# Kernel optimization log

Measured on AMD Instinct MI355X. Metric: run time of the kernel, lower is better.

## Reference

```python
import jax, jax.numpy as jnp
import numpy as np

K = 16  # neighbors


def _knn_idx(pts, k):
    # pts: [B,N,3] -> idx [B,N,K] of k nearest points (self included), unsorted order ok
    sq = jnp.sum(pts * pts, axis=-1)                                  # [B,N]
    d = sq[:, :, None] + sq[:, None, :] - 2.0 * jnp.einsum('bnd,bmd->bnm', pts, pts)
    return jax.lax.top_k(-d, k)[1]                                    # [B,N,K]


def _gather(x, idx):
    # x: [B,N,C], idx: [B,N,K] -> [B,N,K,C]
    return jax.vmap(lambda xb, ib: xb[ib])(x, idx)


def _lin(x, W, b):
    # pointwise (kernel-1 conv / linear): x [...,Cin], W [Cout,Cin]
    return jnp.einsum('...c,oc->...o', x, W) + b


def _local_maxpool(x, idx):
    return jnp.max(_gather(x, idx), axis=2)                           # [B,N,C]


def setup_inputs() -> dict:
    key = jax.random.key(0)
    ks = jax.random.split(key, 24)
    B, N = 8, 4096

    def p(k, shape):
        fan_in = shape[-1]
        return jax.random.normal(k, shape, jnp.float32) * (1.0 / np.sqrt(fan_in))

    z = lambda n: jnp.zeros((n,), jnp.float32)
    return {
        'pts': jax.random.normal(ks[0], (B, N, 3), jnp.float32),
        'w1': p(ks[1], (64, 12)),    'b1': z(64),
        'w2': p(ks[2], (64, 64)),    'b2': z(64),
        'w3': p(ks[3], (64, 64)),    'b3': z(64),
        'lw1': p(ks[4], (64, 64)),   'lb1': z(64),
        'cw1': p(ks[5], (128, 64)),  'cb1': z(128),
        'lw2': p(ks[6], (128, 128)), 'lb2': z(128),
        'cw2': p(ks[7], (1024, 128)),'cb2': z(1024),
        'mw1': p(ks[8], (512, 1024)),'mb1': z(512),
        'mw2': p(ks[9], (512, 512)), 'mb2': z(512),
    }


def reference(pts, w1, b1, w2, b2, w3, b3, lw1, lb1, cw1, cb1,
              lw2, lb2, cw2, cb2, mw1, mb1, mw2, mb2):
    B, N, d = pts.shape
    idx = _knn_idx(pts, K)                                            # [B,N,K]

    # local covariance: gather neighbors, center, outer-product sum
    nb = _gather(pts, idx)                                            # [B,N,K,3]
    nb = nb - jnp.mean(nb, axis=2, keepdims=True)
    cov = jnp.einsum('bnki,bnkj->bnij', nb, nb).reshape(B, N, d * d)  # [B,N,9]
    x = jnp.concatenate([pts, cov], axis=-1)                          # [B,N,12]

    # mlp1 (three 1x1 convs + relu)
    x = jax.nn.relu(_lin(x, w1, b1))
    x = jax.nn.relu(_lin(x, w2, b2))
    x = jax.nn.relu(_lin(x, w3, b3))                                  # [B,N,64]

    # graph layer
    x = _local_maxpool(x, idx)
    x = _lin(x, lw1, lb1)
    x = jax.nn.relu(_lin(x, cw1, cb1))                                # [B,N,128]
    x = _local_maxpool(x, idx)
    x = _lin(x, lw2, lb2)
    x = _lin(x, cw2, cb2)                                             # [B,N,1024]

    # global max pool over points, then mlp2
    x = jnp.max(x, axis=1, keepdims=True)                             # [B,1,1024]
    x = jax.nn.relu(_lin(x, mw1, mb1))
    x = _lin(x, mw2, mb2)                                             # [B,1,512]
    return x
```

## Files before the change

### kernel.cpp

```cpp
#include <hip/hip_runtime.h>

#define NPTS 4096
#define NBATCH 8

typedef __attribute__((ext_vector_type(8))) short short8v;
typedef __attribute__((ext_vector_type(4))) float f32x4;

__device__ __forceinline__ unsigned fenc(float f) {
  unsigned u = __float_as_uint(f);
  return (u & 0x80000000u) ? ~u : (u | 0x80000000u);
}
__device__ __forceinline__ float fdec(unsigned e) {
  unsigned u = (e & 0x80000000u) ? (e ^ 0x80000000u) : ~e;
  return __uint_as_float(u);
}
__device__ __forceinline__ float dot4(float4 a, float4 b) {
  return a.x * b.x + a.y * b.y + a.z * b.z + a.w * b.w;
}
__device__ __forceinline__ unsigned short f2bf(float f) {
  unsigned u = __float_as_uint(f);
  return (unsigned short)((u + 0x7fffu + ((u >> 16) & 1u)) >> 16);
}

__global__ __launch_bounds__(256)
void k_wb(const float* __restrict__ cw2, unsigned short* __restrict__ cw2B) {
  int tid = blockIdx.x * 256 + threadIdx.x;
  int l = tid & 63, ks = (tid >> 6) & 3, nt = tid >> 8;
  int n = nt * 16 + (l & 15);
  int kb = ks * 32 + (l >> 4) * 8;
  const float* src = cw2 + (size_t)n * 128 + kb;
  unsigned short* dst = cw2B + (size_t)tid * 8;
#pragma unroll
  for (int j = 0; j < 8; j++) dst[j] = f2bf(src[j]);
}

__global__ __launch_bounds__(256)
void k_pack(const float* __restrict__ pts, float4* __restrict__ pts4) {
  int i = blockIdx.x * 256 + threadIdx.x;
  float x = pts[3 * i], y = pts[3 * i + 1], z = pts[3 * i + 2];
  pts4[i] = make_float4(x, y, z, x * x + y * y + z * z);
}

__global__ __launch_bounds__(512)
void k_knn(const float4* __restrict__ pts4, int* __restrict__ idxo,
           float* __restrict__ x0) {
  __shared__ float bufd[16][512];
  __shared__ unsigned short bufi[16][512];

  const int b = blockIdx.x >> 6;
  const int ch = blockIdx.x & 63;
  const float4* pb4 = pts4 + (size_t)b * NPTS;

  const int t = threadIdx.x;
  const int tq = t & 63;
  const int seg = __builtin_amdgcn_readfirstlane(t >> 6);
  const int q = ch * 64 + tq;
  const float4 qp = pb4[q];
  const float qs = qp.w;

  float td[16];
  int ti[16];
#pragma unroll
  for (int j = 0; j < 16; j++) { td[j] = 3.0e38f; ti[j] = 0; }
  float worst = 3.0e38f;
  int cnt = 0;

  auto merge = [&]() {
    float bd[16];
    int bi[16];
#pragma unroll
    for (int j = 0; j < 16; j++) {
      bool v = j < cnt;
      float dv = bufd[j][t];
      int iv = (int)bufi[j][t];
      bd[j] = v ? dv : 3.0e38f;
      bi[j] = v ? iv : 0;
    }
    cnt = 0;
#pragma unroll
    for (int k = 2; k <= 16; k <<= 1) {
#pragma unroll
      for (int j = k >> 1; j > 0; j >>= 1) {
#pragma unroll
        for (int i = 0; i < 16; i++) {
          int l = i ^ j;
          if (l > i) {
            bool dir = ((i & k) == 0);
            bool sw = dir ? (bd[i] > bd[l]) : (bd[i] < bd[l]);
            float fd = sw ? bd[l] : bd[i];
            float fl = sw ? bd[i] : bd[l];
            int gd = sw ? bi[l] : bi[i];
            int gl = sw ? bi[i] : bi[l];
            bd[i] = fd; bd[l] = fl; bi[i] = gd; bi[l] = gl;
          }
        }
      }
    }
#pragma unroll
    for (int i = 0; i < 16; i++) {
      int l = 15 - i;
      bool sw = bd[l] < td[i];
      td[i] = sw ? bd[l] : td[i];
      ti[i] = sw ? bi[l] : ti[i];
    }
#pragma unroll
    for (int j = 8; j > 0; j >>= 1) {
#pragma unroll
      for (int i = 0; i < 16; i++) {
        int l = i ^ j;
        if (l > i) {
          bool sw = td[i] > td[l];
          float fd = sw ? td[l] : td[i];
          float fl = sw ? td[i] : td[l];
          int gd = sw ? ti[l] : ti[i];
          int gl = sw ? ti[i] : ti[l];
          td[i] = fd; td[l] = fl; ti[i] = gd; ti[l] = gl;
        }
      }
    }
    worst = td[15];
  };

  const float4* ps = pb4 + seg * 512;
  const int base = seg * 512;
  for (int i0 = 0; i0 < 512; i0 += 8) {
    float4 c[8];
#pragma unroll
    for (int u = 0; u < 8; u++) c[u] = ps[i0 + u];
    float d[8];
#pragma unroll
    for (int u = 0; u < 8; u++)
      d[u] = (qs + c[u].w) - 2.0f * (qp.x * c[u].x + qp.y * c[u].y + qp.z * c[u].z);
#pragma unroll
    for (int u = 0; u < 8; u++) {
      if (d[u] < worst) {
        bufd[cnt][t] = d[u];
        bufi[cnt][t] = (unsigned short)(base + i0 + u);
        cnt++;
      }
      if (u == 3 && __any(cnt >= 13)) merge();
    }
    if (__any(cnt >= 13)) merge();
  }
  if (__any(cnt > 0)) merge();

#pragma unroll
  for (int j = 0; j < 16; j++) { bufd[j][t] = td[j]; bufi[j][t] = (unsigned short)ti[j]; }
  __syncthreads();
  if (t < 64) {
#pragma unroll
    for (int s = 1; s < 8; s++) {
      float bd[16];
      int bi[16];
#pragma unroll
      for (int j = 0; j < 16; j++) {
        bd[j] = bufd[j][t + 64 * s];
        bi[j] = (int)bufi[j][t + 64 * s];
      }
#pragma unroll
      for (int i = 0; i < 16; i++) {
        int l = 15 - i;
        bool sw = bd[l] < td[i];
        td[i] = sw ? bd[l] : td[i];
        ti[i] = sw ? bi[l] : ti[i];
      }
#pragma unroll
      for (int j = 8; j > 0; j >>= 1) {
#pragma unroll
        for (int i = 0; i < 16; i++) {
          int l = i ^ j;
          if (l > i) {
            bool sw2 = td[i] > td[l];
            float fd = sw2 ? td[l] : td[i];
            float fl = sw2 ? td[i] : td[l];
            int gd = sw2 ? ti[l] : ti[i];
            int gl = sw2 ? ti[i] : ti[l];
            td[i] = fd; td[l] = fl; ti[i] = gd; ti[l] = gl;
          }
        }
      }
    }

    float nx[16], ny[16], nz[16];
    float mx = 0.f, my = 0.f, mz = 0.f;
#pragma unroll
    for (int k = 0; k < 16; k++) {
      float4 c = pb4[ti[k]];
      nx[k] = c.x; ny[k] = c.y; nz[k] = c.z;
      mx += c.x; my += c.y; mz += c.z;
    }
    mx *= 0.0625f; my *= 0.0625f; mz *= 0.0625f;
    float c00 = 0, c01 = 0, c02 = 0, c11 = 0, c12 = 0, c22 = 0;
#pragma unroll
    for (int k = 0; k < 16; k++) {
      float dx = nx[k] - mx, dy = ny[k] - my, dz = nz[k] - mz;
      c00 += dx * dx; c01 += dx * dy; c02 += dx * dz;
      c11 += dy * dy; c12 += dy * dz; c22 += dz * dz;
    }
    size_t row = (size_t)b * NPTS + q;
    float* xo = x0 + row * 12;
    xo[0] = qp.x; xo[1] = qp.y; xo[2] = qp.z;
    xo[3] = c00;  xo[4] = c01;  xo[5] = c02;
    xo[6] = c01;  xo[7] = c11;  xo[8] = c12;
    xo[9] = c02;  xo[10] = c12; xo[11] = c22;
    int* io = idxo + row * 16;
#pragma unroll
    for (int k = 0; k < 16; k++) io[k] = ti[k];
  }
}

__global__ __launch_bounds__(128)
void k_mlp1(const float* __restrict__ x0,
            const float* __restrict__ w1, const float* __restrict__ b1,
            const float* __restrict__ w2, const float* __restrict__ b2,
            const float* __restrict__ w3, const float* __restrict__ b3,
            float* __restrict__ h3o) {
  __shared__ float s1[64 * 12], s2[64 * 64], s3[64 * 64];
  __shared__ float sb1[64], sb2[64], sb3[64];
  for (int i = threadIdx.x; i < 64 * 12; i += 128) s1[i] = w1[i];
  for (int i = threadIdx.x; i < 64 * 64; i += 128) { s2[i] = w2[i]; s3[i] = w3[i]; }
  if (threadIdx.x < 64) {
    sb1[threadIdx.x] = b1[threadIdx.x];
    sb2[threadIdx.x] = b2[threadIdx.x];
    sb3[threadIdx.x] = b3[threadIdx.x];
  }
  __syncthreads();

  size_t p = (size_t)blockIdx.x * 128 + threadIdx.x;
  const float4* xv = (const float4*)(x0 + p * 12);
  float4 xa = xv[0], xb = xv[1], xc = xv[2];

  float h[64];
#pragma unroll
  for (int o = 0; o < 64; o++) {
    const float4* wr = (const float4*)(s1 + o * 12);
    float a = sb1[o] + dot4(wr[0], xa) + dot4(wr[1], xb) + dot4(wr[2], xc);
    h[o] = fmaxf(a, 0.f);
  }
  float g[64];
#pragma unroll
  for (int o = 0; o < 64; o++) {
    float a = sb2[o];
    const float4* wr = (const float4*)(s2 + o * 64);
#pragma unroll
    for (int c4 = 0; c4 < 16; c4++) {
      float4 w = wr[c4];
      a += w.x * h[4 * c4] + w.y * h[4 * c4 + 1] + w.z * h[4 * c4 + 2] + w.w * h[4 * c4 + 3];
    }
    g[o] = fmaxf(a, 0.f);
  }
  float* out = h3o + p * 64;
  for (int o = 0; o < 64; o++) {
    float a = sb3[o];
    const float4* wr = (const float4*)(s3 + o * 64);
#pragma unroll
    for (int c4 = 0; c4 < 16; c4++) {
      float4 w = wr[c4];
      a += w.x * g[4 * c4] + w.y * g[4 * c4 + 1] + w.z * g[4 * c4 + 2] + w.w * g[4 * c4 + 3];
    }
    out[o] = fmaxf(a, 0.f);
  }
}

__global__ __launch_bounds__(256)
void k_graph1(const float* __restrict__ h3, const int* __restrict__ idx,
              const float* __restrict__ lw1, const float* __restrict__ lb1,
              const float* __restrict__ cw1, const float* __restrict__ cb1,
              float* __restrict__ z) {
  __shared__ float smc[64][64];
  __shared__ float yc[64][64];

  const int b = blockIdx.x >> 6;
  const int pbase = (blockIdx.x & 63) * 64;
  const int t = threadIdx.x;
  const int pl = t & 63;
  const int cg = __builtin_amdgcn_readfirstlane(t >> 6);

  {
    size_t p = (size_t)b * NPTS + pbase + pl;
    const int* ip = idx + p * 16;
    float mv[16];
#pragma unroll
    for (int c = 0; c < 16; c++) mv[c] = -3.0e38f;
    for (int k = 0; k < 16; k++) {
      const float4* nb = (const float4*)(h3 + (((size_t)b << 12) + ip[k]) * 64 + cg * 16);
#pragma unroll
      for (int c4 = 0; c4 < 4; c4++) {
        float4 v = nb[c4];
        mv[4 * c4]     = fmaxf(mv[4 * c4], v.x);
        mv[4 * c4 + 1] = fmaxf(mv[4 * c4 + 1], v.y);
        mv[4 * c4 + 2] = fmaxf(mv[4 * c4 + 2], v.z);
        mv[4 * c4 + 3] = fmaxf(mv[4 * c4 + 3], v.w);
      }
    }
#pragma unroll
    for (int c = 0; c < 16; c++) smc[cg * 16 + c][pl] = mv[c];
  }
  __syncthreads();

  {
    float m[64];
#pragma unroll
    for (int c = 0; c < 64; c++) m[c] = smc[c][pl];
    for (int j = 0; j < 16; j++) {
      const float* wr = lw1 + (size_t)(cg * 16 + j) * 64;
      float a = lb1[cg * 16 + j];
#pragma unroll
      for (int c = 0; c < 64; c++) a += wr[c] * m[c];
      yc[cg * 16 + j][pl] = a;
    }
  }
  __syncthreads();

  {
    float y[64];
#pragma unroll
    for (int c = 0; c < 64; c++) y[c] = yc[c][pl];
    size_t p = (size_t)b * NPTS + pbase + pl;
    float* zo = z + p * 128 + cg * 32;
    for (int o4 = 0; o4 < 8; o4++) {
      float r[4];
#pragma unroll
      for (int oi = 0; oi < 4; oi++) {
        int o = o4 * 4 + oi;
        const float* wr = cw1 + (size_t)(cg * 32 + o) * 64;
        float a = cb1[cg * 32 + o];
#pragma unroll
        for (int c = 0; c < 64; c++) a += wr[c] * y[c];
        r[oi] = fmaxf(a, 0.f);
      }
      *(float4*)(zo + o4 * 4) = make_float4(r[0], r[1], r[2], r[3]);
    }
  }
}

__global__ __launch_bounds__(256)
void k_graph2(const float* __restrict__ z, const int* __restrict__ idx,
              const float* __restrict__ lw2, const float* __restrict__ lb2,
              const unsigned short* __restrict__ cw2B, const float* __restrict__ cb2,
              unsigned* __restrict__ gacc) {
  __shared__ float smT[128][64];
  __shared__ alignas(16) unsigned short stb[64 * 128];

  const int b = blockIdx.x >> 6;
  const int pbase = (blockIdx.x & 63) * 64;
  const int t = threadIdx.x;

  {
    const int pl = t & 63, cg = t >> 6;
    size_t p = (size_t)b * NPTS + pbase + pl;
    const int* ip = idx + p * 16;
    float mv[32];
#pragma unroll
    for (int c = 0; c < 32; c++) mv[c] = -3.0e38f;
    for (int k = 0; k < 16; k++) {
      const float4* nb = (const float4*)(z + ((size_t)b * NPTS + ip[k]) * 128 + cg * 32);
#pragma unroll
      for (int c4 = 0; c4 < 8; c4++) {
        float4 v = nb[c4];
        mv[4 * c4]     = fmaxf(mv[4 * c4], v.x);
        mv[4 * c4 + 1] = fmaxf(mv[4 * c4 + 1], v.y);
        mv[4 * c4 + 2] = fmaxf(mv[4 * c4 + 2], v.z);
        mv[4 * c4 + 3] = fmaxf(mv[4 * c4 + 3], v.w);
      }
    }
#pragma unroll
    for (int c = 0; c < 32; c++) smT[cg * 32 + c][pl] = mv[c];
  }
  __syncthreads();

  {
    const int pl = t & 63, og = t >> 6;
    float acc[32];
#pragma unroll
    for (int oi = 0; oi < 32; oi++) acc[oi] = lb2[og * 32 + oi];
    for (int cb = 0; cb < 4; cb++) {
      float mr[32];
#pragma unroll
      for (int j = 0; j < 32; j++) mr[j] = smT[cb * 32 + j][pl];
#pragma unroll
      for (int oi = 0; oi < 32; oi++) {
        const float4* wr = (const float4*)(lw2 + (size_t)(og * 32 + oi) * 128 + cb * 32);
#pragma unroll
        for (int j4 = 0; j4 < 8; j4++) {
          float4 w = wr[j4];
          acc[oi] += w.x * mr[4 * j4] + w.y * mr[4 * j4 + 1] + w.z * mr[4 * j4 + 2] + w.w * mr[4 * j4 + 3];
        }
      }
    }
#pragma unroll
    for (int e = 0; e < 4; e++) {
      short8v v;
#pragma unroll
      for (int j = 0; j < 8; j++) v[j] = (short)f2bf(acc[e * 8 + j]);
      int bc = (og * 64 + e * 16) ^ ((pl & 7) << 4);
      *(short8v*)((char*)stb + pl * 256 + bc) = v;
    }
  }
  __syncthreads();

  {
    const int wv = t >> 6;
    const int l = t & 63;
    const int lr = l & 15;
    const int lg = l >> 4;
    short8v a[4][4];
#pragma unroll
    for (int mt = 0; mt < 4; mt++)
#pragma unroll
      for (int ks = 0; ks < 4; ks++) {
        int row = mt * 16 + lr;
        int bc = (ks * 64 + lg * 16) ^ ((row & 7) << 4);
        a[mt][ks] = *(const short8v*)((const char*)stb + row * 256 + bc);
      }
    const short8v* cb8 = (const short8v*)cw2B;
    float bmax[16];
#pragma unroll
    for (int i = 0; i < 16; i++) {
      const int nt = wv * 16 + i;
      short8v bf[4];
#pragma unroll
      for (int ks = 0; ks < 4; ks++) bf[ks] = cb8[(nt * 4 + ks) * 64 + l];
      float mm = -3.0e38f;
#pragma unroll
      for (int mt = 0; mt < 4; mt++) {
        f32x4 acc = {0.f, 0.f, 0.f, 0.f};
#pragma unroll
        for (int ks = 0; ks < 4; ks++)
          acc = __builtin_amdgcn_mfma_f32_16x16x32_bf16(a[mt][ks], bf[ks], acc, 0, 0, 0);
        mm = fmaxf(mm, fmaxf(fmaxf(acc[0], acc[1]), fmaxf(acc[2], acc[3])));
      }
      mm = fmaxf(mm, __shfl_xor(mm, 16));
      mm = fmaxf(mm, __shfl_xor(mm, 32));
      bmax[i] = mm + cb2[nt * 16 + lr];
    }
    if (l < 16) {
#pragma unroll
      for (int i = 0; i < 16; i++)
        atomicMax(&gacc[b * 1024 + (wv * 16 + i) * 16 + l], fenc(bmax[i]));
    }
  }
}

__global__ __launch_bounds__(512)
void k_head(const unsigned* __restrict__ gacc,
            const float* __restrict__ mw1, const float* __restrict__ mb1,
            const float* __restrict__ mw2, const float* __restrict__ mb2,
            float* __restrict__ out) {
  __shared__ float g[1024];
  __shared__ float h[512];
  const int b = blockIdx.x, t = threadIdx.x;
  for (int i = t; i < 1024; i += 512) g[i] = fdec(gacc[b * 1024 + i]);
  __syncthreads();
  float a = mb1[t];
  const float4* wr = (const float4*)(mw1 + (size_t)t * 1024);
  const float4* gv = (const float4*)g;
#pragma unroll 8
  for (int c4 = 0; c4 < 256; c4++) a += dot4(wr[c4], gv[c4]);
  h[t] = fmaxf(a, 0.f);
  __syncthreads();
  float a2 = mb2[t];
  const float4* wr2 = (const float4*)(mw2 + (size_t)t * 512);
  const float4* hv = (const float4*)h;
#pragma unroll 8
  for (int c4 = 0; c4 < 128; c4++) a2 += dot4(wr2[c4], hv[c4]);
  out[(size_t)b * 512 + t] = a2;
}

extern "C" void kernel_launch(void* const* d_in, const int* in_sizes, int n_in,
                              void* d_out, int out_size, void* d_ws, size_t ws_size,
                              hipStream_t stream) {
  const float* pts = (const float*)d_in[0];
  const float* w1  = (const float*)d_in[1];
  const float* b1  = (const float*)d_in[2];
  const float* w2  = (const float*)d_in[3];
  const float* b2  = (const float*)d_in[4];
  const float* w3  = (const float*)d_in[5];
  const float* b3  = (const float*)d_in[6];
  const float* lw1 = (const float*)d_in[7];
  const float* lb1 = (const float*)d_in[8];
  const float* cw1 = (const float*)d_in[9];
  const float* cb1 = (const float*)d_in[10];
  const float* lw2 = (const float*)d_in[11];
  const float* lb2 = (const float*)d_in[12];
  const float* cw2 = (const float*)d_in[13];
  const float* cb2 = (const float*)d_in[14];
  const float* mw1 = (const float*)d_in[15];
  const float* mb1 = (const float*)d_in[16];
  const float* mw2 = (const float*)d_in[17];
  const float* mb2 = (const float*)d_in[18];

  char* ws = (char*)d_ws;
  int*      idx  = (int*)(ws);
  float*    x0   = (float*)(ws + 2097152);
  float*    h3   = (float*)(ws + 2097152 + 1572864);
  float*    z    = (float*)(ws + 2097152 + 1572864 + 8388608);
  unsigned* gacc = (unsigned*)(ws + 28835840);
  unsigned short* cw2B = (unsigned short*)(ws + 28835840 + 32768);
  float4*   pts4 = (float4*)(ws + 28835840 + 32768 + 262144);

  hipMemsetAsync(gacc, 0, NBATCH * 1024 * sizeof(unsigned), stream);
  k_wb<<<64, 256, 0, stream>>>(cw2, cw2B);
  k_pack<<<(NBATCH * NPTS) / 256, 256, 0, stream>>>(pts, pts4);
  k_knn<<<NBATCH * (NPTS / 64), 512, 0, stream>>>(pts4, idx, x0);
  k_mlp1<<<(NBATCH * NPTS) / 128, 128, 0, stream>>>(x0, w1, b1, w2, b2, w3, b3, h3);
  k_graph1<<<NBATCH * 64, 256, 0, stream>>>(h3, idx, lw1, lb1, cw1, cb1, z);
  k_graph2<<<NBATCH * (NPTS / 64), 256, 0, stream>>>(z, idx, lw2, lb2, cw2B, cb2, gacc);
  k_head<<<NBATCH, 512, 0, stream>>>(gacc, mw1, mb1, mw2, mb2, (float*)d_out);
}
```

Baseline: 507.0 us.

## Restructure mlp1 into block-cooperative layers and split head across more blocks

The per-point MLP1 kernel now has each block handle 64 points, with 4 waves each computing 16 output channels. Intermediate activations are staged in shared memory and weights are read through wave-uniform global loads, which cuts per-thread register arrays and redundant LDS weight copies. The MLP head, previously 8 blocks each doing a serial 1024-long dot product per thread, is split into two kernels over 64 blocks each. These use transposed weights for coalesced reads and an 8-way partial-sum reduction. This raises parallelism in the tiny head stage but adds two transpose launches and an extra head launch on every call.

```diff
diff --git a/kernel.cpp b/kernel.cpp
--- a/kernel.cpp
+++ b/kernel.cpp
@@ -39,6 +39,13 @@
   int i = blockIdx.x * 256 + threadIdx.x;
   float x = pts[3 * i], y = pts[3 * i + 1], z = pts[3 * i + 2];
   pts4[i] = make_float4(x, y, z, x * x + y * y + z * z);
+}
+
+__global__ __launch_bounds__(256)
+void k_trh(const float* __restrict__ src, float* __restrict__ dst, int cin) {
+  int idx = blockIdx.x * 256 + threadIdx.x;
+  int c = idx >> 9, o = idx & 511;
+  dst[idx] = src[o * cin + c];
 }
 
 __global__ __launch_bounds__(512)
@@ -209,56 +216,76 @@
   }
 }
 
-__global__ __launch_bounds__(128)
+__global__ __launch_bounds__(256)
 void k_mlp1(const float* __restrict__ x0,
             const float* __restrict__ w1, const float* __restrict__ b1,
             const float* __restrict__ w2, const float* __restrict__ b2,
             const float* __restrict__ w3, const float* __restrict__ b3,
             float* __restrict__ h3o) {
-  __shared__ float s1[64 * 12], s2[64 * 64], s3[64 * 64];
-  __shared__ float sb1[64], sb2[64], sb3[64];
-  for (int i = threadIdx.x; i < 64 * 12; i += 128) s1[i] = w1[i];
-  for (int i = threadIdx.x; i < 64 * 64; i += 128) { s2[i] = w2[i]; s3[i] = w3[i]; }
-  if (threadIdx.x < 64) {
-    sb1[threadIdx.x] = b1[threadIdx.x];
-    sb2[threadIdx.x] = b2[threadIdx.x];
-    sb3[threadIdx.x] = b3[threadIdx.x];
-  }
-  __syncthreads();
-
-  size_t p = (size_t)blockIdx.x * 128 + threadIdx.x;
-  const float4* xv = (const float4*)(x0 + p * 12);
-  float4 xa = xv[0], xb = xv[1], xc = xv[2];
-
-  float h[64];
-#pragma unroll
-  for (int o = 0; o < 64; o++) {
-    const float4* wr = (const float4*)(s1 + o * 12);
-    float a = sb1[o] + dot4(wr[0], xa) + dot4(wr[1], xb) + dot4(wr[2], xc);
-    h[o] = fmaxf(a, 0.f);
-  }
-  float g[64];
-#pragma unroll
-  for (int o = 0; o < 64; o++) {
-    float a = sb2[o];
-    const float4* wr = (const float4*)(s2 + o * 64);
-#pragma unroll
-    for (int c4 = 0; c4 < 16; c4++) {
-      float4 w = wr[c4];
-      a += w.x * h[4 * c4] + w.y * h[4 * c4 + 1] + w.z * h[4 * c4 + 2] + w.w * h[4 * c4 + 3];
-    }
-    g[o] = fmaxf(a, 0.f);
-  }
-  float* out = h3o + p * 64;
-  for (int o = 0; o < 64; o++) {
-    float a = sb3[o];
-    const float4* wr = (const float4*)(s3 + o * 64);
-#pragma unroll
-    for (int c4 = 0; c4 < 16; c4++) {
-      float4 w = wr[c4];
-      a += w.x * g[4 * c4] + w.y * g[4 * c4 + 1] + w.z * g[4 * c4 + 2] + w.w * g[4 * c4 + 3];
-    }
-    out[o] = fmaxf(a, 0.f);
+  __shared__ float xs[12][64];
+  __shared__ float h1[64][64];
+  __shared__ float h2[64][64];
+
+  const int b = blockIdx.x >> 6;
+  const int pbase = (blockIdx.x & 63) * 64;
+  const int t = threadIdx.x;
+  const int pl = t & 63;
+  const int cg = __builtin_amdgcn_readfirstlane(t >> 6);
+
+  {
+    const float* xt = x0 + ((size_t)b * NPTS + pbase) * 12;
+    for (int e = t; e < 768; e += 256) xs[e % 12][e / 12] = xt[e];
+  }
+  __syncthreads();
+
+  {
+    float x[12];
+#pragma unroll
+    for (int c = 0; c < 12; c++) x[c] = xs[c][pl];
+    for (int j = 0; j < 16; j++) {
+      int o = cg * 16 + j;
+      const float* wr = w1 + (size_t)o * 12;
+      float a = b1[o];
+#pragma unroll
+      for (int c = 0; c < 12; c++) a += wr[c] * x[c];
+      h1[o][pl] = fmaxf(a, 0.f);
+    }
+  }
+  __syncthreads();
+
+  {
+    float m[64];
+#pragma unroll
+    for (int c = 0; c < 64; c++) m[c] = h1[c][pl];
+    for (int j = 0; j < 16; j++) {
+      int o = cg * 16 + j;
+      const float* wr = w2 + (size_t)o * 64;
+      float a = b2[o];
+#pragma unroll
+      for (int c = 0; c < 64; c++) a += wr[c] * m[c];
+      h2[o][pl] = fmaxf(a, 0.f);
+    }
+  }
+  __syncthreads();
+
+  {
+    float m[64];
+#pragma unroll
+    for (int c = 0; c < 64; c++) m[c] = h2[c][pl];
+    float* out = h3o + ((size_t)b * NPTS + pbase + pl) * 64 + cg * 16;
+    for (int j4 = 0; j4 < 4; j4++) {
+      float r[4];
+#pragma unroll
+      for (int ji = 0; ji < 4; ji++) {
+        int o = cg * 16 + j4 * 4 + ji;
+        const float* wr = w3 + (size_t)o * 64;
+        float a = b3[o];
+#pragma unroll
+        for (int c = 0; c < 64; c++) a += wr[c] * m[c];
+        r[ji] = fmaxf(a, 0.f);
+      }
+      *(float4*)(out + j4 * 4) = make_float4(r[0], r[1], r[2], r[3]);
+    }
   }
 }
 
@@ -443,28 +470,55 @@
 }
 
 __global__ __launch_bounds__(512)
-void k_head(const unsigned* __restrict__ gacc,
-            const float* __restrict__ mw1, const float* __restrict__ mb1,
-            const float* __restrict__ mw2, const float* __restrict__ mb2,
-            float* __restrict__ out) {
-  __shared__ float g[1024];
-  __shared__ float h[512];
-  const int b = blockIdx.x, t = threadIdx.x;
-  for (int i = t; i < 1024; i += 512) g[i] = fdec(gacc[b * 1024 + i]);
-  __syncthreads();
-  float a = mb1[t];
-  const float4* wr = (const float4*)(mw1 + (size_t)t * 1024);
-  const float4* gv = (const float4*)g;
+void k_head1(const unsigned* __restrict__ gacc, const float* __restrict__ mw1T,
+             const float* __restrict__ mb1, float* __restrict__ hbuf) {
+  __shared__ float gs[1024];
+  __shared__ float psum[8][64];
+  const int b = blockIdx.x >> 3;
+  const int og = blockIdx.x & 7;
+  const int t = threadIdx.x;
+  const int o = t & 63;
+  const int w = __builtin_amdgcn_readfirstlane(t >> 6);
+  for (int i = t; i < 1024; i += 512) gs[i] = fdec(gacc[b * 1024 + i]);
+  __syncthreads();
+  float a = 0.f;
+  const float* wp = mw1T + (size_t)(w * 128) * 512 + og * 64 + o;
 #pragma unroll 8
-  for (int c4 = 0; c4 < 256; c4++) a += dot4(wr[c4], gv[c4]);
-  h[t] = fmaxf(a, 0.f);
-  __syncthreads();
-  float a2 = mb2[t];
-  const float4* wr2 = (const float4*)(mw2 + (size_t)t * 512);
-  const float4* hv = (const float4*)h;
+  for (int c = 0; c < 128; c++) a += wp[c * 512] * gs[w * 128 + c];
+  psum[w][o] = a;
+  __syncthreads();
+  if (t < 64) {
+    float s = mb1[og * 64 + t];
+#pragma unroll
+    for (int ww = 0; ww < 8; ww++) s += psum[ww][t];
+    hbuf[b * 512 + og * 64 + t] = fmaxf(s, 0.f);
+  }
+}
+
+__global__ __launch_bounds__(512)
+void k_head2(const float* __restrict__ hbuf, const float* __restrict__ mw2T,
+             const float* __restrict__ mb2, float* __restrict__ out) {
+  __shared__ float hs[512];
+  __shared__ float psum[8][64];
+  const int b = blockIdx.x >> 3;
+  const int og = blockIdx.x & 7;
+  const int t = threadIdx.x;
+  const int o = t & 63;
+  const int w = __builtin_amdgcn_readfirstlane(t >> 6);
+  if (t < 512) hs[t] = hbuf[b * 512 + t];
+  __syncthreads();
+  float a = 0.f;
+  const float* wp = mw2T + (size_t)(w * 64) * 512 + og * 64 + o;
 #pragma unroll 8
-  for (int c4 = 0; c4 < 128; c4++) a2 += dot4(wr2[c4], hv[c4]);
-  out[(size_t)b * 512 + t] = a2;
+  for (int c = 0; c < 64; c++) a += wp[c * 512] * hs[w * 64 + c];
+  psum[w][o] = a;
+  __syncthreads();
+  if (t < 64) {
+    float s = mb2[og * 64 + t];
+#pragma unroll
+    for (int ww = 0; ww < 8; ww++) s += psum[ww][t];
+    out[(size_t)b * 512 + og * 64 + t] = s;
+  }
 }
 
 extern "C" void kernel_launch(void* const* d_in, const int* in_sizes, int n_in,
@@ -498,13 +552,19 @@
   unsigned* gacc = (unsigned*)(ws + 28835840);
   unsigned short* cw2B = (unsigned short*)(ws + 28835840 + 32768);
   float4*   pts4 = (float4*)(ws + 28835840 + 32768 + 262144);
+  float*    mw1T = (float*)(ws + 29655040);
+  float*    mw2T = (float*)(ws + 29655040 + 2097152);
+  float*    hbuf = (float*)(ws + 29655040 + 2097152 + 1048576);
 
   hipMemsetAsync(gacc, 0, NBATCH * 1024 * sizeof(unsigned), stream);
   k_wb<<<64, 256, 0, stream>>>(cw2, cw2B);
   k_pack<<<(NBATCH * NPTS) / 256, 256, 0, stream>>>(pts, pts4);
+  k_trh<<<2048, 256, 0, stream>>>(mw1, mw1T, 1024);
+  k_trh<<<1024, 256, 0, stream>>>(mw2, mw2T, 512);
   k_knn<<<NBATCH * (NPTS / 64), 512, 0, stream>>>(pts4, idx, x0);
-  k_mlp1<<<(NBATCH * NPTS) / 128, 128, 0, stream>>>(x0, w1, b1, w2, b2, w3, b3, h3);
+  k_mlp1<<<NBATCH * 64, 256, 0, stream>>>(x0, w1, b1, w2, b2, w3, b3, h3);
   k_graph1<<<NBATCH * 64, 256, 0, stream>>>(h3, idx, lw1, lb1, cw1, cb1, z);
   k_graph2<<<NBATCH * (NPTS / 64), 256, 0, stream>>>(z, idx, lw2, lb2, cw2B, cb2, gacc);
-  k_head<<<NBATCH, 512, 0, stream>>>(gacc, mw1, mb1, mw2, mb2, (float*)d_out);
-}
+  k_head1<<<NBATCH * 8, 512, 0, stream>>>(gacc, mw1T, mb1, hbuf);
+  k_head2<<<NBATCH * 8, 512, 0, stream>>>(hbuf, mw2T, mb2, (float*)d_out);
+}
```

Result: faster. 410.1 us (-19.1%).
